# Kernel tuning notes

Hardware: AMD Instinct MI355X
Metric: run time of the kernel (lower is better)

Reference implementation:

```python
import jax, jax.numpy as jnp
import numpy as np

INNER_DIM = 1024

def setup_inputs() -> dict:
    key = jax.random.key(0)
    ks = jax.random.split(key, 6)
    b, n, d = 4, 4096, 1024
    s = 0.02
    return {
        "x": jax.random.normal(ks[0], (b, n, d), jnp.float32),
        "y": jax.random.normal(ks[1], (b, n, d), jnp.float32),
        "Wq": jax.random.normal(ks[2], (INNER_DIM, d), jnp.float32) * s,
        "Wk": jax.random.normal(ks[3], (INNER_DIM, d), jnp.float32) * s,
        "Wv": jax.random.normal(ks[4], (INNER_DIM, d), jnp.float32) * s,
        "Wo": jax.random.normal(ks[5], (d, INNER_DIM), jnp.float32) * s,
        "bo": jnp.zeros((d,), jnp.float32),
    }

def reference(x, y, Wq, Wk, Wv, Wo, bo):
    # torch Linear: out = inp @ W.T ; weights stored [out_dim, in_dim]
    q = jnp.einsum('bnd,ed->bne', y, Wq)  # queries come from y
    k = jnp.einsum('bnd,ed->bne', x, Wk)
    v = jnp.einsum('bnd,ed->bne', x, Wv)
    dk = 1.0 / jnp.sqrt(jnp.asarray(INNER_DIM, q.dtype))  # full inner_dim, not per-head
    alpha = jnp.einsum('bie,bje->bij', q, k) * dk  # [b, n, n] full score matrix
    alpha = jax.nn.softmax(alpha, axis=-1)
    # NOTE: original masked_fill is a no-op (result discarded), so no causal mask.
    ctx = jnp.einsum('bij,bje->bie', alpha, v)
    return jnp.einsum('bie,de->bid', ctx, Wo) + bo
```

## Files before the change

kernel.cpp:

```cpp
#include <hip/hip_runtime.h>
#include <stdint.h>

typedef __attribute__((ext_vector_type(8))) short s16x8;
typedef __attribute__((ext_vector_type(4))) float f32x4;

__device__ __forceinline__ unsigned short f2bf(float f) {
    union { float f; uint32_t u; } c; c.f = f;
    uint32_t u = c.u + 0x7FFFu + ((c.u >> 16) & 1u);
    return (unsigned short)(u >> 16);
}

__device__ __forceinline__ float bf2f(unsigned int u16) {
    union { uint32_t u; float f; } c; c.u = u16 << 16;
    return c.f;
}

__device__ __forceinline__ void load_lds16(const unsigned short* g, unsigned short* l) {
    __builtin_amdgcn_global_load_lds(
        (const __attribute__((address_space(1))) char*)(uintptr_t)g,
        (__attribute__((address_space(3))) char*)(uint32_t)(uintptr_t)l,
        16, 0, 0);
}

template <bool OUT_BF16, bool HAS_BIAS, bool EXP_OUT>
__global__ __launch_bounds__(256, 4)
void gemm_bt(const unsigned short* __restrict__ A, long lda, long sA,
             const unsigned short* __restrict__ B, long ldb, long sB,
             void* __restrict__ C, long ldc, long sC,
             const float* __restrict__ bias, int K, float scale)
{
    __shared__ __align__(16) unsigned short As[128 * 64];
    __shared__ __align__(16) unsigned short Bs[128 * 64];

    const unsigned gx = gridDim.x, gy = gridDim.y;
    const unsigned lin = blockIdx.x + gx * blockIdx.y;
    const unsigned g   = lin & 7u;
    const unsigned j   = lin >> 3;
    const unsigned bxs = j & (gx - 1u);
    const unsigned bys = g * (gy >> 3) + j / gx;

    const int tid  = threadIdx.x;
    const int wave = tid >> 6;
    const int lane = tid & 63;
    const int wm = wave & 1;
    const int wn = wave >> 1;

    const unsigned short* Ap = A + (long)blockIdx.z * sA + (long)bys * 128 * lda;
    const unsigned short* Bp = B + (long)blockIdx.z * sB + (long)bxs * 128 * ldb;

    const int lrow = lane >> 3;
    const int lk   = ((lane & 7) ^ lrow) * 8;
    const int cl   = lane & 15;
    const int qd   = lane >> 4;
    const int sw   = (cl & 7) * 8;

    f32x4 acc[4][4];
#pragma unroll
    for (int i = 0; i < 4; ++i)
#pragma unroll
        for (int j2 = 0; j2 < 4; ++j2)
            acc[i][j2] = f32x4{0.f, 0.f, 0.f, 0.f};

    for (int k0 = 0; k0 < K; k0 += 64) {
#pragma unroll
        for (int c2 = 0; c2 < 4; ++c2) {
            const int  c   = wave * 4 + c2;
            const long row = c * 8 + lrow;
            load_lds16(Ap + row * lda + k0 + lk, &As[c * 512]);
            load_lds16(Bp + row * ldb + k0 + lk, &Bs[c * 512]);
        }
        __syncthreads();
#pragma unroll
        for (int kk = 0; kk < 64; kk += 32) {
            s16x8 af[4], bf[4];
#pragma unroll
            for (int i = 0; i < 4; ++i) {
                af[i] = *(const s16x8*)&As[(wm * 64 + i * 16 + cl) * 64 + ((kk + qd * 8) ^ sw)];
                bf[i] = *(const s16x8*)&Bs[(wn * 64 + i * 16 + cl) * 64 + ((kk + qd * 8) ^ sw)];
            }
#pragma unroll
            for (int i = 0; i < 4; ++i)
#pragma unroll
                for (int j2 = 0; j2 < 4; ++j2)
                    acc[i][j2] = __builtin_amdgcn_mfma_f32_16x16x32_bf16(
                        af[i], bf[j2], acc[i][j2], 0, 0, 0);
        }
        __syncthreads();
    }

    const long row0 = (long)bys * 128 + wm * 64;
    const long col0 = (long)bxs * 128 + wn * 64;
    const long zC   = (long)blockIdx.z * sC;
#pragma unroll
    for (int i = 0; i < 4; ++i) {
#pragma unroll
        for (int j2 = 0; j2 < 4; ++j2) {
            const long c = col0 + j2 * 16 + cl;
            float badd = 0.f;
            if constexpr (HAS_BIAS) badd = bias[c];
            const long rb = row0 + i * 16 + qd * 4;
#pragma unroll
            for (int r = 0; r < 4; ++r) {
                float v = acc[i][j2][r] * scale + badd;
                if constexpr (EXP_OUT) v = __expf(v);
                const long idx = zC + (rb + r) * ldc + c;
                if constexpr (OUT_BF16) ((unsigned short*)C)[idx] = f2bf(v);
                else                    ((float*)C)[idx] = v;
            }
        }
    }
}

__global__ __launch_bounds__(256, 4)
void gemm_pv4(const unsigned short* __restrict__ p0,
              const unsigned short* __restrict__ p1,
              const unsigned short* __restrict__ p2,
              const unsigned short* __restrict__ p3,
              const unsigned short* __restrict__ Bv, long ldb, long sB,
              unsigned short* __restrict__ C, long ldc, long sC,
              const float* __restrict__ rowdiv, int K, long lda)
{
    __shared__ __align__(16) unsigned short As[128 * 64];
    __shared__ __align__(16) unsigned short Bs[128 * 64];

    const unsigned gx = gridDim.x, gy = gridDim.y;
    const unsigned lin = blockIdx.x + gx * blockIdx.y;
    const unsigned g   = lin & 7u;
    const unsigned j   = lin >> 3;
    const unsigned bxs = j & (gx - 1u);
    const unsigned bys = g * (gy >> 3) + j / gx;

    const int z = blockIdx.z;
    const unsigned short* A = (z == 0) ? p0 : (z == 1) ? p1 : (z == 2) ? p2 : p3;

    const int tid  = threadIdx.x;
    const int wave = tid >> 6;
    const int lane = tid & 63;
    const int wm = wave & 1;
    const int wn = wave >> 1;

    const unsigned short* Ap = A + (long)bys * 128 * lda;
    const unsigned short* Bp = Bv + (long)z * sB + (long)bxs * 128 * ldb;

    const int lrow = lane >> 3;
    const int lk   = ((lane & 7) ^ lrow) * 8;
    const int cl   = lane & 15;
    const int qd   = lane >> 4;
    const int sw   = (cl & 7) * 8;

    f32x4 acc[4][4];
#pragma unroll
    for (int i = 0; i < 4; ++i)
#pragma unroll
        for (int j2 = 0; j2 < 4; ++j2)
            acc[i][j2] = f32x4{0.f, 0.f, 0.f, 0.f};

    for (int k0 = 0; k0 < K; k0 += 64) {
#pragma unroll
        for (int c2 = 0; c2 < 4; ++c2) {
            const int  c   = wave * 4 + c2;
            const long row = c * 8 + lrow;
            load_lds16(Ap + row * lda + k0 + lk, &As[c * 512]);
            load_lds16(Bp + row * ldb + k0 + lk, &Bs[c * 512]);
        }
        __syncthreads();
#pragma unroll
        for (int kk = 0; kk < 64; kk += 32) {
            s16x8 af[4], bf[4];
#pragma unroll
            for (int i = 0; i < 4; ++i) {
                af[i] = *(const s16x8*)&As[(wm * 64 + i * 16 + cl) * 64 + ((kk + qd * 8) ^ sw)];
                bf[i] = *(const s16x8*)&Bs[(wn * 64 + i * 16 + cl) * 64 + ((kk + qd * 8) ^ sw)];
            }
#pragma unroll
            for (int i = 0; i < 4; ++i)
#pragma unroll
                for (int j2 = 0; j2 < 4; ++j2)
                    acc[i][j2] = __builtin_amdgcn_mfma_f32_16x16x32_bf16(
                        af[i], bf[j2], acc[i][j2], 0, 0, 0);
        }
        __syncthreads();
    }

    const long row0 = (long)bys * 128 + wm * 64;
    const long col0 = (long)bxs * 128 + wn * 64;
    const long zC   = (long)z * sC;
    const float* rd = rowdiv + (long)z * 4096;
#pragma unroll
    for (int i = 0; i < 4; ++i) {
        const long rb = row0 + i * 16 + qd * 4;
        float rinv[4];
#pragma unroll
        for (int r = 0; r < 4; ++r) rinv[r] = 1.f / rd[rb + r];
#pragma unroll
        for (int j2 = 0; j2 < 4; ++j2) {
            const long c = col0 + j2 * 16 + cl;
#pragma unroll
            for (int r = 0; r < 4; ++r)
                C[zC + (rb + r) * ldc + c] = f2bf(acc[i][j2][r] * rinv[r]);
        }
    }
}

__global__ __launch_bounds__(256)
void rowsum4(const unsigned short* __restrict__ p0,
             const unsigned short* __restrict__ p1,
             const unsigned short* __restrict__ p2,
             const unsigned short* __restrict__ p3,
             float* __restrict__ rs)
{
    const unsigned row = blockIdx.x;
    const unsigned b = row >> 12;
    const unsigned short* P = (b == 0) ? p0 : (b == 1) ? p1 : (b == 2) ? p2 : p3;
    const long r = row & 4095u;
    const int tid = threadIdx.x, lane = tid & 63, wave = tid >> 6;

    const uint4* src = (const uint4*)(P + r * 4096);
    uint4 u0 = src[tid], u1 = src[tid + 256];
    float s = 0.f;
    {
        const unsigned* a = (const unsigned*)&u0;
        const unsigned* c = (const unsigned*)&u1;
#pragma unroll
        for (int i = 0; i < 4; ++i) {
            s += bf2f(a[i] & 0xFFFFu) + bf2f(a[i] >> 16);
            s += bf2f(c[i] & 0xFFFFu) + bf2f(c[i] >> 16);
        }
    }
#pragma unroll
    for (int off = 32; off > 0; off >>= 1) s += __shfl_xor(s, off);
    __shared__ float red[4];
    if (lane == 0) red[wave] = s;
    __syncthreads();
    if (tid == 0) rs[row] = red[0] + red[1] + red[2] + red[3];
}

__global__ __launch_bounds__(256)
void cast2_bf16(const float* __restrict__ s0, unsigned short* __restrict__ d0,
                const float* __restrict__ s1, unsigned short* __restrict__ d1)
{
    const float*    in  = blockIdx.y ? s1 : s0;
    unsigned short* out = blockIdx.y ? d1 : d0;
    const long i = ((long)blockIdx.x * 256 + threadIdx.x) * 4;
    const float4 v = *(const float4*)(in + i);
    ushort4 o;
    o.x = f2bf(v.x); o.y = f2bf(v.y); o.z = f2bf(v.z); o.w = f2bf(v.w);
    *(ushort4*)(out + i) = o;
}

__global__ __launch_bounds__(256)
void cast4_bf16(const float* __restrict__ s0, unsigned short* __restrict__ d0,
                const float* __restrict__ s1, unsigned short* __restrict__ d1,
                const float* __restrict__ s2, unsigned short* __restrict__ d2,
                const float* __restrict__ s3, unsigned short* __restrict__ d3)
{
    const float* in; unsigned short* out;
    switch (blockIdx.y) {
        case 0: in = s0; out = d0; break;
        case 1: in = s1; out = d1; break;
        case 2: in = s2; out = d2; break;
        default: in = s3; out = d3; break;
    }
    const long i = ((long)blockIdx.x * 256 + threadIdx.x) * 4;
    const float4 v = *(const float4*)(in + i);
    ushort4 o;
    o.x = f2bf(v.x); o.y = f2bf(v.y); o.z = f2bf(v.z); o.w = f2bf(v.w);
    *(ushort4*)(out + i) = o;
}

extern "C" void kernel_launch(void* const* d_in, const int* in_sizes, int n_in,
                              void* d_out, int out_size, void* d_ws, size_t ws_size,
                              hipStream_t stream)
{
    (void)in_sizes; (void)n_in; (void)out_size;
    const float* x  = (const float*)d_in[0];
    const float* y  = (const float*)d_in[1];
    const float* Wq = (const float*)d_in[2];
    const float* Wk = (const float*)d_in[3];
    const float* Wv = (const float*)d_in[4];
    const float* Wo = (const float*)d_in[5];
    const float* bo = (const float*)d_in[6];
    float* out = (float*)d_out;

    const long N = 4096, D = 1024;
    const long NB = N * D;
    const long NN = N * N;
    const size_t MiB = 1ull << 20;
    const float dk = 0.03125f;
    char* w = (char*)d_ws;

    if (ws_size >= 200 * MiB) {
        unsigned short* Xb  = (unsigned short*)(w);
        unsigned short* Yb  = (unsigned short*)(w + 32 * MiB);
        unsigned short* Qb  = (unsigned short*)(w + 64 * MiB);
        unsigned short* Kb  = (unsigned short*)(w + 96 * MiB);
        unsigned short* VT  = (unsigned short*)(w + 128 * MiB);
        unsigned short* Wqb = (unsigned short*)(w + 192 * MiB);
        unsigned short* Wkb = (unsigned short*)(w + 194 * MiB);
        unsigned short* Wvb = (unsigned short*)(w + 196 * MiB);
        unsigned short* Wob = (unsigned short*)(w + 198 * MiB);
        unsigned short* P0  = (unsigned short*)(w);
        unsigned short* P1  = (unsigned short*)(w + 32 * MiB);
        unsigned short* P2  = (unsigned short*)(w + 160 * MiB);
        unsigned short* P3  = (unsigned short*)d_out;
        unsigned short* Cx  = (unsigned short*)(w + 64 * MiB);
        float*          rsm = (float*)(w + 192 * MiB);

        cast2_bf16<<<dim3(16384, 2), dim3(256), 0, stream>>>(x, Xb, y, Yb);
        cast4_bf16<<<dim3(1024, 4),  dim3(256), 0, stream>>>(
            Wq, Wqb, Wk, Wkb, Wv, Wvb, Wo, Wob);

        gemm_bt<true, false, false><<<dim3(8, 128, 2), dim3(256), 0, stream>>>(
            Yb, D, (long)(Xb - Yb), Wqb, D, (long)(Wkb - Wqb),
            Qb, D, (long)(Kb - Qb), nullptr, D, 1.f);
        gemm_bt<true, false, false><<<dim3(32, 8, 4), dim3(256), 0, stream>>>(
            Wvb, D, 0, Xb, D, NB, VT, N, NB, nullptr, D, 1.f);

        gemm_bt<true, false, true><<<dim3(32, 32, 2), dim3(256), 0, stream>>>(
            Qb, D, NB, Kb, D, NB, P0, N, (long)(P1 - P0), nullptr, D, dk);
        gemm_bt<true, false, true><<<dim3(32, 32, 2), dim3(256), 0, stream>>>(
            Qb + 2 * NB, D, NB, Kb + 2 * NB, D, NB,
            P2, N, (long)(P3 - P2), nullptr, D, dk);
        rowsum4<<<dim3(16384), dim3(256), 0, stream>>>(P0, P1, P2, P3, rsm);

        gemm_pv4<<<dim3(8, 32, 4), dim3(256), 0, stream>>>(
            P0, P1, P2, P3, VT, N, NB, Cx, D, NB, rsm, (int)N, N);
        gemm_bt<false, true, false><<<dim3(8, 128, 1), dim3(256), 0, stream>>>(
            Cx, D, 0, Wob, D, 0, out, D, 0, bo, D, 1.f);
    } else if (ws_size >= 104 * MiB) {
        unsigned short* Wqb = (unsigned short*)(w);
        unsigned short* Wkb = (unsigned short*)(w + 2 * MiB);
        unsigned short* Wvb = (unsigned short*)(w + 4 * MiB);
        unsigned short* Wob = (unsigned short*)(w + 6 * MiB);
        unsigned short* xb  = (unsigned short*)(w + 8 * MiB);
        unsigned short* yb  = (unsigned short*)(w + 16 * MiB);
        unsigned short* Qb  = (unsigned short*)(w + 24 * MiB);
        unsigned short* Kb  = (unsigned short*)(w + 32 * MiB);
        unsigned short* VTb = (unsigned short*)(w + 40 * MiB);
        unsigned short* Cxb = (unsigned short*)(w + 48 * MiB);
        unsigned short* Pb  = (unsigned short*)(w + 56 * MiB);
        float*          rsm = (float*)(w + 88 * MiB);

        cast4_bf16<<<dim3(1024, 4), dim3(256), 0, stream>>>(
            Wq, Wqb, Wk, Wkb, Wv, Wvb, Wo, Wob);

        for (int b = 0; b < 4; ++b) {
            cast2_bf16<<<dim3(4096, 2), dim3(256), 0, stream>>>(
                x + b * NB, xb, y + b * NB, yb);
            gemm_bt<true, false, false><<<dim3(8, 32, 1), dim3(256), 0, stream>>>(
                yb, D, 0, Wqb, D, 0, Qb, D, 0, nullptr, D, 1.f);
            gemm_bt<true, false, false><<<dim3(8, 32, 1), dim3(256), 0, stream>>>(
                xb, D, 0, Wkb, D, 0, Kb, D, 0, nullptr, D, 1.f);
            gemm_bt<true, false, false><<<dim3(32, 8, 1), dim3(256), 0, stream>>>(
                Wvb, D, 0, xb, D, 0, VTb, N, 0, nullptr, D, 1.f);
            gemm_bt<true, false, true><<<dim3(32, 32, 1), dim3(256), 0, stream>>>(
                Qb, D, 0, Kb, D, 0, Pb, N, 0, nullptr, D, dk);
            rowsum4<<<dim3(4096), dim3(256), 0, stream>>>(Pb, Pb, Pb, Pb, rsm);
            gemm_pv4<<<dim3(8, 32, 1), dim3(256), 0, stream>>>(
                Pb, Pb, Pb, Pb, VTb, N, 0, Cxb, D, 0, rsm, (int)N, N);
            gemm_bt<false, true, false><<<dim3(8, 32, 1), dim3(256), 0, stream>>>(
                Cxb, D, 0, Wob, D, 0, out + b * NB, D, 0, bo, D, 1.f);
        }
    }
}
```

Baseline: 622.8 us.

## Use 256x256 tiles with double-buffered LDS pipelining in all GEMMs

Replaces the 128x128 single-buffered GEMM kernels with 256x256-tile kernels using 512 threads. The K-loop double-buffers LDS, issuing the next tile's global-to-LDS loads in stages between MFMA groups, with manual waitcnt/barrier and setprio. This is meant to hide load latency and raise arithmetic intensity per byte loaded. In exchange it uses 128KB of LDS and 128 accumulator registers per thread, so occupancy drops, and small grids may underfill the CUs.

```diff
diff --git a/kernel.cpp b/kernel.cpp
--- a/kernel.cpp
+++ b/kernel.cpp
@@ -22,86 +22,142 @@
         16, 0, 0);
 }
 
+__device__ __forceinline__ void gemm256_core(
+    const unsigned short* __restrict__ Ap, long lda,
+    const unsigned short* __restrict__ Bp, long ldb,
+    int nt, unsigned short* As, unsigned short* Bs, f32x4 (*acc)[2])
+{
+    const int tid  = threadIdx.x;
+    const int wv   = tid >> 6;
+    const int lane = tid & 63;
+    const int cl   = lane & 15;
+    const int qd   = lane >> 4;
+
+    const int ch0 = (wv << 7) + lane, ch1 = ch0 + 64;
+    const int r0 = ch0 >> 3, r1 = ch1 >> 3;
+    const long gA0 = (long)r0 * lda + (((ch0 & 7) ^ (r0 & 7)) << 3);
+    const long gA1 = (long)r1 * lda + (((ch1 & 7) ^ (r1 & 7)) << 3);
+    const long gB0 = (long)r0 * ldb + (((ch0 & 7) ^ (r0 & 7)) << 3);
+    const long gB1 = (long)r1 * ldb + (((ch1 & 7) ^ (r1 & 7)) << 3);
+    const int  d0  = (wv << 10);
+    const int  d1  = d0 + 512;
+
+    const int k0off = (((qd    ) ^ (cl & 7)) << 3) + cl * 64;
+    const int k1off = (((4 + qd) ^ (cl & 7)) << 3) + cl * 64;
+
+    load_lds16(Bp + gB0, Bs + d0);
+    load_lds16(Bp + gB1, Bs + d1);
+    load_lds16(Bp + 128 * ldb + gB0, Bs + 8192 + d0);
+    load_lds16(Bp + 128 * ldb + gB1, Bs + 8192 + d1);
+    load_lds16(Ap + gA0, As + d0);
+    load_lds16(Ap + gA1, As + d1);
+    load_lds16(Ap + 128 * lda + gA0, As + 8192 + d0);
+    load_lds16(Ap + 128 * lda + gA1, As + 8192 + d1);
+    asm volatile("s_waitcnt vmcnt(2)" ::: "memory");
+    asm volatile("s_barrier" ::: "memory");
+
+    for (int t = 0; t < nt; ++t) {
+        const unsigned short* Ab = As + ((t & 1) << 14);
+        const unsigned short* Bb = Bs + ((t & 1) << 14);
+        unsigned short* An = As + (((t + 1) & 1) << 14);
+        unsigned short* Bn = Bs + (((t + 1) & 1) << 14);
+        const long kn   = (long)(t + 1) << 6;
+        const bool more = (t + 1) < nt;
+        s16x8 bfr[2][2];
+#pragma unroll
+        for (int p = 0; p < 4; ++p) {
+            s16x8 af[4][2];
+#pragma unroll
+            for (int i = 0; i < 4; ++i) {
+                af[i][0] = *(const s16x8*)&Ab[(p * 4 + i) * 1024 + k0off];
+                af[i][1] = *(const s16x8*)&Ab[(p * 4 + i) * 1024 + k1off];
+            }
+            if (p == 0) {
+#pragma unroll
+                for (int j = 0; j < 2; ++j) {
+                    bfr[j][0] = *(const s16x8*)&Bb[(wv * 2 + j) * 1024 + k0off];
+                    bfr[j][1] = *(const s16x8*)&Bb[(wv * 2 + j) * 1024 + k1off];
+                }
+            }
+            if (more) {
+                if (p == 0)      { load_lds16(Bp + kn + gB0, Bn + d0);
+                                   load_lds16(Bp + kn + gB1, Bn + d1); }
+                else if (p == 1) { load_lds16(Bp + 128 * ldb + kn + gB0, Bn + 8192 + d0);
+                                   load_lds16(Bp + 128 * ldb + kn + gB1, Bn + 8192 + d1); }
+                else if (p == 2) { load_lds16(Ap + kn + gA0, An + d0);
+                                   load_lds16(Ap + kn + gA1, An + d1); }
+                else             { load_lds16(Ap + 128 * lda + kn + gA0, An + 8192 + d0);
+                                   load_lds16(Ap + 128 * lda + kn + gA1, An + 8192 + d1); }
+            }
+            __builtin_amdgcn_s_setprio(1);
+#pragma unroll
+            for (int i = 0; i < 4; ++i)
+#pragma unroll
+                for (int j = 0; j < 2; ++j) {
+                    acc[p * 4 + i][j] = __builtin_amdgcn_mfma_f32_16x16x32_bf16(
+                        af[i][0], bfr[j][0], acc[p * 4 + i][j], 0, 0, 0);
+                    acc[p * 4 + i][j] = __builtin_amdgcn_mfma_f32_16x16x32_bf16(
+                        af[i][1], bfr[j][1], acc[p * 4 + i][j], 0, 0, 0);
+                }
+            __builtin_amdgcn_s_setprio(0);
+            if (p == 1) {
+                if (more) asm volatile("s_waitcnt vmcnt(4)" ::: "memory");
+                else      asm volatile("s_waitcnt vmcnt(0)" ::: "memory");
+            } else if (p == 3) {
+                if (more) asm volatile("s_waitcnt vmcnt(2)" ::: "memory");
+            }
+            asm volatile("s_barrier" ::: "memory");
+        }
+    }
+}
+
 template <bool OUT_BF16, bool HAS_BIAS, bool EXP_OUT>
-__global__ __launch_bounds__(256, 4)
-void gemm_bt(const unsigned short* __restrict__ A, long lda, long sA,
+__global__ __launch_bounds__(512, 2)
+void gemm256(const unsigned short* __restrict__ A, long lda, long sA,
              const unsigned short* __restrict__ B, long ldb, long sB,
              void* __restrict__ C, long ldc, long sC,
              const float* __restrict__ bias, int K, float scale)
 {
-    __shared__ __align__(16) unsigned short As[128 * 64];
-    __shared__ __align__(16) unsigned short Bs[128 * 64];
+    __shared__ __align__(16) unsigned short As[2 * 16384];
+    __shared__ __align__(16) unsigned short Bs[2 * 16384];
 
     const unsigned gx = gridDim.x, gy = gridDim.y;
     const unsigned lin = blockIdx.x + gx * blockIdx.y;
-    const unsigned g   = lin & 7u;
-    const unsigned j   = lin >> 3;
-    const unsigned bxs = j & (gx - 1u);
-    const unsigned bys = g * (gy >> 3) + j / gx;
-
-    const int tid  = threadIdx.x;
-    const int wave = tid >> 6;
-    const int lane = tid & 63;
-    const int wm = wave & 1;
-    const int wn = wave >> 1;
-
-    const unsigned short* Ap = A + (long)blockIdx.z * sA + (long)bys * 128 * lda;
-    const unsigned short* Bp = B + (long)blockIdx.z * sB + (long)bxs * 128 * ldb;
-
-    const int lrow = lane >> 3;
-    const int lk   = ((lane & 7) ^ lrow) * 8;
-    const int cl   = lane & 15;
-    const int qd   = lane >> 4;
-    const int sw   = (cl & 7) * 8;
-
-    f32x4 acc[4][4];
-#pragma unroll
-    for (int i = 0; i < 4; ++i)
-#pragma unroll
-        for (int j2 = 0; j2 < 4; ++j2)
-            acc[i][j2] = f32x4{0.f, 0.f, 0.f, 0.f};
-
-    for (int k0 = 0; k0 < K; k0 += 64) {
-#pragma unroll
-        for (int c2 = 0; c2 < 4; ++c2) {
-            const int  c   = wave * 4 + c2;
-            const long row = c * 8 + lrow;
-            load_lds16(Ap + row * lda + k0 + lk, &As[c * 512]);
-            load_lds16(Bp + row * ldb + k0 + lk, &Bs[c * 512]);
-        }
-        __syncthreads();
-#pragma unroll
-        for (int kk = 0; kk < 64; kk += 32) {
-            s16x8 af[4], bf[4];
-#pragma unroll
-            for (int i = 0; i < 4; ++i) {
-                af[i] = *(const s16x8*)&As[(wm * 64 + i * 16 + cl) * 64 + ((kk + qd * 8) ^ sw)];
-                bf[i] = *(const s16x8*)&Bs[(wn * 64 + i * 16 + cl) * 64 + ((kk + qd * 8) ^ sw)];
-            }
-#pragma unroll
-            for (int i = 0; i < 4; ++i)
-#pragma unroll
-                for (int j2 = 0; j2 < 4; ++j2)
-                    acc[i][j2] = __builtin_amdgcn_mfma_f32_16x16x32_bf16(
-                        af[i], bf[j2], acc[i][j2], 0, 0, 0);
-        }
-        __syncthreads();
-    }
-
-    const long row0 = (long)bys * 128 + wm * 64;
-    const long col0 = (long)bxs * 128 + wn * 64;
+    unsigned bxs, bys;
+    if ((gy & 7u) == 0u) {
+        const unsigned g = lin & 7u, j = lin >> 3;
+        bxs = j & (gx - 1u);
+        bys = g * (gy >> 3) + j / gx;
+    } else { bxs = blockIdx.x; bys = blockIdx.y; }
+
+    const unsigned short* Ap = A + (long)blockIdx.z * sA + (long)bys * 256 * lda;
+    const unsigned short* Bp = B + (long)blockIdx.z * sB + (long)bxs * 256 * ldb;
+
+    f32x4 acc[16][2];
+#pragma unroll
+    for (int i = 0; i < 16; ++i) {
+        acc[i][0] = f32x4{0.f, 0.f, 0.f, 0.f};
+        acc[i][1] = f32x4{0.f, 0.f, 0.f, 0.f};
+    }
+
+    gemm256_core(Ap, lda, Bp, ldb, K >> 6, As, Bs, acc);
+
+    const int wv = threadIdx.x >> 6;
+    const int cl = threadIdx.x & 15, qd = (threadIdx.x & 63) >> 4;
+    const long row0 = (long)bys * 256;
+    const long col0 = (long)bxs * 256 + wv * 32;
     const long zC   = (long)blockIdx.z * sC;
 #pragma unroll
-    for (int i = 0; i < 4; ++i) {
-#pragma unroll
-        for (int j2 = 0; j2 < 4; ++j2) {
-            const long c = col0 + j2 * 16 + cl;
-            float badd = 0.f;
-            if constexpr (HAS_BIAS) badd = bias[c];
+    for (int j = 0; j < 2; ++j) {
+        const long c = col0 + j * 16 + cl;
+        float badd = 0.f;
+        if constexpr (HAS_BIAS) badd = bias[c];
+#pragma unroll
+        for (int i = 0; i < 16; ++i) {
             const long rb = row0 + i * 16 + qd * 4;
 #pragma unroll
             for (int r = 0; r < 4; ++r) {
-                float v = acc[i][j2][r] * scale + badd;
+                float v = acc[i][j][r] * scale + badd;
                 if constexpr (EXP_OUT) v = __expf(v);
                 const long idx = zC + (rb + r) * ldc + c;
                 if constexpr (OUT_BF16) ((unsigned short*)C)[idx] = f2bf(v);
@@ -111,93 +167,60 @@
     }
 }
 
-__global__ __launch_bounds__(256, 4)
-void gemm_pv4(const unsigned short* __restrict__ p0,
-              const unsigned short* __restrict__ p1,
-              const unsigned short* __restrict__ p2,
-              const unsigned short* __restrict__ p3,
-              const unsigned short* __restrict__ Bv, long ldb, long sB,
-              unsigned short* __restrict__ C, long ldc, long sC,
-              const float* __restrict__ rowdiv, int K, long lda)
-{
-    __shared__ __align__(16) unsigned short As[128 * 64];
-    __shared__ __align__(16) unsigned short Bs[128 * 64];
+__global__ __launch_bounds__(512, 2)
+void gemm256_pv4(const unsigned short* __restrict__ p0,
+                 const unsigned short* __restrict__ p1,
+                 const unsigned short* __restrict__ p2,
+                 const unsigned short* __restrict__ p3,
+                 const unsigned short* __restrict__ Bv, long ldb, long sB,
+                 unsigned short* __restrict__ C, long ldc, long sC,
+                 const float* __restrict__ rowdiv, int K, long lda)
+{
+    __shared__ __align__(16) unsigned short As[2 * 16384];
+    __shared__ __align__(16) unsigned short Bs[2 * 16384];
 
     const unsigned gx = gridDim.x, gy = gridDim.y;
     const unsigned lin = blockIdx.x + gx * blockIdx.y;
-    const unsigned g   = lin & 7u;
-    const unsigned j   = lin >> 3;
-    const unsigned bxs = j & (gx - 1u);
-    const unsigned bys = g * (gy >> 3) + j / gx;
+    unsigned bxs, bys;
+    if ((gy & 7u) == 0u) {
+        const unsigned g = lin & 7u, j = lin >> 3;
+        bxs = j & (gx - 1u);
+        bys = g * (gy >> 3) + j / gx;
+    } else { bxs = blockIdx.x; bys = blockIdx.y; }
 
     const int z = blockIdx.z;
     const unsigned short* A = (z == 0) ? p0 : (z == 1) ? p1 : (z == 2) ? p2 : p3;
 
-    const int tid  = threadIdx.x;
-    const int wave = tid >> 6;
-    const int lane = tid & 63;
-    const int wm = wave & 1;
-    const int wn = wave >> 1;
-
-    const unsigned short* Ap = A + (long)bys * 128 * lda;
-    const unsigned short* Bp = Bv + (long)z * sB + (long)bxs * 128 * ldb;
-
-    const int lrow = lane >> 3;
-    const int lk   = ((lane & 7) ^ lrow) * 8;
-    const int cl   = lane & 15;
-    const int qd   = lane >> 4;
-    const int sw   = (cl & 7) * 8;
-
-    f32x4 acc[4][4];
-#pragma unroll
-    for (int i = 0; i < 4; ++i)
-#pragma unroll
-        for (int j2 = 0; j2 < 4; ++j2)
-            acc[i][j2] = f32x4{0.f, 0.f, 0.f, 0.f};
-
-    for (int k0 = 0; k0 < K; k0 += 64) {
-#pragma unroll
-        for (int c2 = 0; c2 < 4; ++c2) {
-            const int  c   = wave * 4 + c2;
-            const long row = c * 8 + lrow;
-            load_lds16(Ap + row * lda + k0 + lk, &As[c * 512]);
-            load_lds16(Bp + row * ldb + k0 + lk, &Bs[c * 512]);
-        }
-        __syncthreads();
-#pragma unroll
-        for (int kk = 0; kk < 64; kk += 32) {
-            s16x8 af[4], bf[4];
-#pragma unroll
-            for (int i = 0; i < 4; ++i) {
-                af[i] = *(const s16x8*)&As[(wm * 64 + i * 16 + cl) * 64 + ((kk + qd * 8) ^ sw)];
-                bf[i] = *(const s16x8*)&Bs[(wn * 64 + i * 16 + cl) * 64 + ((kk + qd * 8) ^ sw)];
-            }
-#pragma unroll
-            for (int i = 0; i < 4; ++i)
-#pragma unroll
-                for (int j2 = 0; j2 < 4; ++j2)
-                    acc[i][j2] = __builtin_amdgcn_mfma_f32_16x16x32_bf16(
-                        af[i], bf[j2], acc[i][j2], 0, 0, 0);
-        }
-        __syncthreads();
-    }
-
-    const long row0 = (long)bys * 128 + wm * 64;
-    const long col0 = (long)bxs * 128 + wn * 64;
+    const unsigned short* Ap = A + (long)bys * 256 * lda;
+    const unsigned short* Bp = Bv + (long)z * sB + (long)bxs * 256 * ldb;
+
+    f32x4 acc[16][2];
+#pragma unroll
+    for (int i = 0; i < 16; ++i) {
+        acc[i][0] = f32x4{0.f, 0.f, 0.f, 0.f};
+        acc[i][1] = f32x4{0.f, 0.f, 0.f, 0.f};
+    }
+
+    gemm256_core(Ap, lda, Bp, ldb, K >> 6, As, Bs, acc);
+
+    const int wv = threadIdx.x >> 6;
+    const int cl = threadIdx.x & 15, qd = (threadIdx.x & 63) >> 4;
+    const long row0 = (long)bys * 256;
+    const long col0 = (long)bxs * 256 + wv * 32;
     const long zC   = (long)z * sC;
     const float* rd = rowdiv + (long)z * 4096;
 #pragma unroll
-    for (int i = 0; i < 4; ++i) {
+    for (int i = 0; i < 16; ++i) {
         const long rb = row0 + i * 16 + qd * 4;
         float rinv[4];
 #pragma unroll
         for (int r = 0; r < 4; ++r) rinv[r] = 1.f / rd[rb + r];
 #pragma unroll
-        for (int j2 = 0; j2 < 4; ++j2) {
-            const long c = col0 + j2 * 16 + cl;
+        for (int j = 0; j < 2; ++j) {
+            const long c = col0 + j * 16 + cl;
 #pragma unroll
             for (int r = 0; r < 4; ++r)
-                C[zC + (rb + r) * ldc + c] = f2bf(acc[i][j2][r] * rinv[r]);
+                C[zC + (rb + r) * ldc + c] = f2bf(acc[i][j][r] * rinv[r]);
         }
     }
 }
@@ -284,7 +307,6 @@
 
     const long N = 4096, D = 1024;
     const long NB = N * D;
-    const long NN = N * N;
     const size_t MiB = 1ull << 20;
     const float dk = 0.03125f;
     char* w = (char*)d_ws;
@@ -310,23 +332,23 @@
         cast4_bf16<<<dim3(1024, 4),  dim3(256), 0, stream>>>(
             Wq, Wqb, Wk, Wkb, Wv, Wvb, Wo, Wob);
 
-        gemm_bt<true, false, false><<<dim3(8, 128, 2), dim3(256), 0, stream>>>(
+        gemm256<true, false, false><<<dim3(4, 64, 2), dim3(512), 0, stream>>>(
             Yb, D, (long)(Xb - Yb), Wqb, D, (long)(Wkb - Wqb),
-            Qb, D, (long)(Kb - Qb), nullptr, D, 1.f);
-        gemm_bt<true, false, false><<<dim3(32, 8, 4), dim3(256), 0, stream>>>(
-            Wvb, D, 0, Xb, D, NB, VT, N, NB, nullptr, D, 1.f);
-
-        gemm_bt<true, false, true><<<dim3(32, 32, 2), dim3(256), 0, stream>>>(
-            Qb, D, NB, Kb, D, NB, P0, N, (long)(P1 - P0), nullptr, D, dk);
-        gemm_bt<true, false, true><<<dim3(32, 32, 2), dim3(256), 0, stream>>>(
+            Qb, D, (long)(Kb - Qb), nullptr, (int)D, 1.f);
+        gemm256<true, false, false><<<dim3(16, 4, 4), dim3(512), 0, stream>>>(
+            Wvb, D, 0, Xb, D, NB, VT, N, NB, nullptr, (int)D, 1.f);
+
+        gemm256<true, false, true><<<dim3(16, 16, 2), dim3(512), 0, stream>>>(
+            Qb, D, NB, Kb, D, NB, P0, N, (long)(P1 - P0), nullptr, (int)D, dk);
+        gemm256<true, false, true><<<dim3(16, 16, 2), dim3(512), 0, stream>>>(
             Qb + 2 * NB, D, NB, Kb + 2 * NB, D, NB,
-            P2, N, (long)(P3 - P2), nullptr, D, dk);
+            P2, N, (long)(P3 - P2), nullptr, (int)D, dk);
         rowsum4<<<dim3(16384), dim3(256), 0, stream>>>(P0, P1, P2, P3, rsm);
 
-        gemm_pv4<<<dim3(8, 32, 4), dim3(256), 0, stream>>>(
+        gemm256_pv4<<<dim3(4, 16, 4), dim3(512), 0, stream>>>(
             P0, P1, P2, P3, VT, N, NB, Cx, D, NB, rsm, (int)N, N);
-        gemm_bt<false, true, false><<<dim3(8, 128, 1), dim3(256), 0, stream>>>(
-            Cx, D, 0, Wob, D, 0, out, D, 0, bo, D, 1.f);
+        gemm256<false, true, false><<<dim3(4, 64, 1), dim3(512), 0, stream>>>(
+            Cx, D, 0, Wob, D, 0, out, D, 0, bo, (int)D, 1.f);
     } else if (ws_size >= 104 * MiB) {
         unsigned short* Wqb = (unsigned short*)(w);
         unsigned short* Wkb = (unsigned short*)(w + 2 * MiB);
@@ -347,19 +369,19 @@
         for (int b = 0; b < 4; ++b) {
             cast2_bf16<<<dim3(4096, 2), dim3(256), 0, stream>>>(
                 x + b * NB, xb, y + b * NB, yb);
-            gemm_bt<true, false, false><<<dim3(8, 32, 1), dim3(256), 0, stream>>>(
-                yb, D, 0, Wqb, D, 0, Qb, D, 0, nullptr, D, 1.f);
-            gemm_bt<true, false, false><<<dim3(8, 32, 1), dim3(256), 0, stream>>>(
-                xb, D, 0, Wkb, D, 0, Kb, D, 0, nullptr, D, 1.f);
-            gemm_bt<true, false, false><<<dim3(32, 8, 1), dim3(256), 0, stream>>>(
-                Wvb, D, 0, xb, D, 0, VTb, N, 0, nullptr, D, 1.f);
-            gemm_bt<true, false, true><<<dim3(32, 32, 1), dim3(256), 0, stream>>>(
-                Qb, D, 0, Kb, D, 0, Pb, N, 0, nullptr, D, dk);
+            gemm256<true, false, false><<<dim3(4, 16, 1), dim3(512), 0, stream>>>(
+                yb, D, 0, Wqb, D, 0, Qb, D, 0, nullptr, (int)D, 1.f);
+            gemm256<true, false, false><<<dim3(4, 16, 1), dim3(512), 0, stream>>>(
+                xb, D, 0, Wkb, D, 0, Kb, D, 0, nullptr, (int)D, 1.f);
+            gemm256<true, false, false><<<dim3(16, 4, 1), dim3(512), 0, stream>>>(
+                Wvb, D, 0, xb, D, 0, VTb, N, 0, nullptr, (int)D, 1.f);
+            gemm256<true, false, true><<<dim3(16, 16, 1), dim3(512), 0, stream>>>(
+                Qb, D, 0, Kb, D, 0, Pb, N, 0, nullptr, (int)D, dk);
             rowsum4<<<dim3(4096), dim3(256), 0, stream>>>(Pb, Pb, Pb, Pb, rsm);
-            gemm_pv4<<<dim3(8, 32, 1), dim3(256), 0, stream>>>(
+            gemm256_pv4<<<dim3(4, 16, 1), dim3(512), 0, stream>>>(
                 Pb, Pb, Pb, Pb, VTb, N, 0, Cxb, D, 0, rsm, (int)N, N);
-            gemm_bt<false, true, false><<<dim3(8, 32, 1), dim3(256), 0, stream>>>(
-                Cxb, D, 0, Wob, D, 0, out + b * NB, D, 0, bo, D, 1.f);
-        }
-    }
-}
+            gemm256<false, true, false><<<dim3(4, 16, 1), dim3(512), 0, stream>>>(
+                Cxb, D, 0, Wob, D, 0, out + b * NB, D, 0, bo, (int)D, 1.f);
+        }
+    }
+}
```

After: 615.4 us. No clear change (-1.2%).
